# Performance work log

Hardware: AMD Instinct MI355X
Metric: run time of the kernel (lower is better)

Reference implementation:

```python
import jax, jax.numpy as jnp
import numpy as np

EMB = 1024
NH = 16
HD = EMB // NH
FF = 4 * EMB
B, T = 2, 2048
LN_EPS = 1e-5


def setup_inputs() -> dict:
    key = jax.random.key(0)
    ks = jax.random.split(key, 16)
    s = 0.02
    return {
        "x": jax.random.normal(ks[0], (B, T, EMB), jnp.float32),
        "wq": jax.random.normal(ks[1], (EMB, EMB), jnp.float32) * s,
        "bq": jnp.zeros((EMB,), jnp.float32),
        "wk": jax.random.normal(ks[2], (EMB, EMB), jnp.float32) * s,
        "bk": jnp.zeros((EMB,), jnp.float32),
        "wv": jax.random.normal(ks[3], (EMB, EMB), jnp.float32) * s,
        "bv": jnp.zeros((EMB,), jnp.float32),
        "wo": jax.random.normal(ks[4], (EMB, EMB), jnp.float32) * s,
        "bo": jnp.zeros((EMB,), jnp.float32),
        "w1": jax.random.normal(ks[5], (EMB, FF), jnp.float32) * s,
        "b1": jnp.zeros((FF,), jnp.float32),
        "w2": jax.random.normal(ks[6], (FF, EMB), jnp.float32) * s,
        "b2": jnp.zeros((EMB,), jnp.float32),
        "ln1_g": jnp.ones((EMB,), jnp.float32),
        "ln1_b": jnp.zeros((EMB,), jnp.float32),
        "ln2_g": jnp.ones((EMB,), jnp.float32),
        "ln2_b": jnp.zeros((EMB,), jnp.float32),
        "alpha_attn": jnp.float32(0.5),
        "alpha_ff": jnp.float32(0.5),
    }


def _layernorm(x, g, b):
    mu = jnp.mean(x, axis=-1, keepdims=True)
    var = jnp.var(x, axis=-1, keepdims=True)
    return (x - mu) * jax.lax.rsqrt(var + LN_EPS) * g + b


def reference(x, wq, bq, wk, bk, wv, bv, wo, bo, w1, b1, w2, b2,
              ln1_g, ln1_b, ln2_g, ln2_b, alpha_attn, alpha_ff):
    residual = x
    x_ = _layernorm(x, ln1_g, ln1_b)
    # [B,T,E] -> [B,H,T,D]
    def heads(y):
        return y.reshape(B, T, NH, HD).transpose(0, 2, 1, 3)
    q = heads(x_ @ wq + bq)
    k = heads(x_ @ wk + bk)
    v = heads(x_ @ wv + bv)
    scores = jnp.einsum("bhqd,bhkd->bhqk", q, k) / np.sqrt(HD).astype(np.float32)
    causal = jnp.tril(jnp.ones((T, T), dtype=bool))
    scores = jnp.where(causal, scores, -jnp.inf)
    attn = jax.nn.softmax(scores, axis=-1)  # dropout is identity in eval mode
    out = jnp.einsum("bhqk,bhkd->bhqd", attn, v)
    out = out.transpose(0, 2, 1, 3).reshape(B, T, EMB)
    out = out @ wo + bo
    x = residual + alpha_attn * out
    x2 = _layernorm(x, ln2_g, ln2_b)
    ff = jax.nn.gelu(x2 @ w1 + b1, approximate=False) @ w2 + b2
    return x + alpha_ff * ff
```

## Files before the change

### kernel.cpp

```cpp
#include <hip/hip_runtime.h>
#include <cmath>

#define EMB 1024
#define NH 16
#define HD 64
#define FF_DIM 4096
#define BB 2
#define TT 2048
#define NTOK (BB * TT)
#define QKVS 3072
#define SC2F 0.18033688011112042f

typedef _Float16 f16x8 __attribute__((ext_vector_type(8)));
typedef _Float16 f16x4 __attribute__((ext_vector_type(4)));
typedef float f32x4 __attribute__((ext_vector_type(4)));

__device__ __forceinline__ float gelu_fast(float x) {
    float u = x * (1.f + 0.044715f * x * x);
    float e = exp2f(u * 2.302118751f);
    return x - x / (e + 1.f);
}

template <typename TIN>
__global__ __launch_bounds__(256) void ln_kernel(const TIN* __restrict__ xin,
                                                 _Float16* __restrict__ out,
                                                 const float* __restrict__ g,
                                                 const float* __restrict__ bv) {
    int tid = threadIdx.x;
    size_t base = (size_t)blockIdx.x * EMB;
    float v[4];
#pragma unroll
    for (int i = 0; i < 4; ++i) v[i] = (float)xin[base + i * 256 + tid];
    float s = v[0] + v[1] + v[2] + v[3];
    float ss = v[0] * v[0] + v[1] * v[1] + v[2] * v[2] + v[3] * v[3];
#pragma unroll
    for (int off = 32; off > 0; off >>= 1) {
        s += __shfl_down(s, off);
        ss += __shfl_down(ss, off);
    }
    __shared__ float red[8];
    int wave = tid >> 6;
    if ((tid & 63) == 0) { red[wave] = s; red[4 + wave] = ss; }
    __syncthreads();
    s = red[0] + red[1] + red[2] + red[3];
    ss = red[4] + red[5] + red[6] + red[7];
    float mu = s * (1.0f / EMB);
    float var = ss * (1.0f / EMB) - mu * mu;
    float rstd = rsqrtf(var + 1e-5f);
#pragma unroll
    for (int i = 0; i < 4; ++i) {
        int idx = i * 256 + tid;
        float y = (v[i] - mu) * rstd * g[idx] + bv[idx];
        out[base + idx] = (_Float16)y;
    }
}

__global__ __launch_bounds__(256) void prep0_kernel(const float* __restrict__ x,
                                                    _Float16* __restrict__ xn,
                                                    const float* __restrict__ ln1_g,
                                                    const float* __restrict__ ln1_b,
                                                    const float* __restrict__ wq,
                                                    const float* __restrict__ wk,
                                                    const float* __restrict__ wv,
                                                    const float* __restrict__ wo,
                                                    const float* __restrict__ bq,
                                                    const float* __restrict__ bk,
                                                    const float* __restrict__ bv,
                                                    _Float16* __restrict__ wqkvT,
                                                    _Float16* __restrict__ woT,
                                                    float* __restrict__ qkvbias) {
    __shared__ float tile[32][33];
    int blk = blockIdx.x;
    int tid = threadIdx.x;
    if (blk >= 4108) {
        size_t base = (size_t)(blk - 4108) * EMB;
        float v[4];
#pragma unroll
        for (int i = 0; i < 4; ++i) v[i] = x[base + i * 256 + tid];
        float s = v[0] + v[1] + v[2] + v[3];
        float ss = v[0] * v[0] + v[1] * v[1] + v[2] * v[2] + v[3] * v[3];
#pragma unroll
        for (int off = 32; off > 0; off >>= 1) {
            s += __shfl_down(s, off);
            ss += __shfl_down(ss, off);
        }
        float* red = &tile[0][0];
        int wave = tid >> 6;
        if ((tid & 63) == 0) { red[wave] = s; red[4 + wave] = ss; }
        __syncthreads();
        s = red[0] + red[1] + red[2] + red[3];
        ss = red[4] + red[5] + red[6] + red[7];
        float mu = s * (1.0f / EMB);
        float var = ss * (1.0f / EMB) - mu * mu;
        float rstd = rsqrtf(var + 1e-5f);
#pragma unroll
        for (int i = 0; i < 4; ++i) {
            int idx = i * 256 + tid;
            xn[base + idx] = (_Float16)((v[i] - mu) * rstd * ln1_g[idx] + ln1_b[idx]);
        }
        return;
    }
    if (blk >= 4096) {
        int i = (blk - 4096) * 256 + tid;
        qkvbias[i] = i < 1024 ? bq[i] : (i < 2048 ? bk[i - 1024] : bv[i - 2048]);
        return;
    }
    const float* W;
    _Float16* Wt;
    int t = blk & 1023;
    int z = blk >> 10;
    if (z == 0) { W = wq; Wt = wqkvT; }
    else if (z == 1) { W = wk; Wt = wqkvT + 1024 * 1024; }
    else if (z == 2) { W = wv; Wt = wqkvT + 2 * 1024 * 1024; }
    else { W = wo; Wt = woT; }
    int bx = (t & 31) * 32, by = (t >> 5) * 32;
    int tx = tid & 31, ty = tid >> 5;
#pragma unroll
    for (int i = 0; i < 32; i += 8)
        tile[ty + i][tx] = W[(size_t)(by + ty + i) * EMB + bx + tx];
    __syncthreads();
#pragma unroll
    for (int i = 0; i < 32; i += 8)
        Wt[(size_t)(bx + ty + i) * EMB + by + tx] = (_Float16)tile[tx][ty + i];
}

__global__ __launch_bounds__(256) void prep2_kernel(const float* __restrict__ w1,
                                                    const float* __restrict__ w2,
                                                    _Float16* __restrict__ w1T,
                                                    _Float16* __restrict__ w2T) {
    int b = blockIdx.x;
    const float* W;
    _Float16* Wt;
    int K, N, t;
    if (b < 4096) { W = w1; Wt = w1T; K = 1024; N = 4096; t = b; }
    else { W = w2; Wt = w2T; K = 4096; N = 1024; t = b - 4096; }
    int ntx = N >> 5;
    int bx = (t % ntx) * 32, by = (t / ntx) * 32;
    __shared__ float tile[32][33];
    int tx = threadIdx.x & 31, ty = threadIdx.x >> 5;
#pragma unroll
    for (int i = 0; i < 32; i += 8)
        tile[ty + i][tx] = W[(size_t)(by + ty + i) * N + bx + tx];
    __syncthreads();
#pragma unroll
    for (int i = 0; i < 32; i += 8)
        Wt[(size_t)(bx + ty + i) * K + by + tx] = (_Float16)tile[tx][ty + i];
}

__global__ __launch_bounds__(256) void vT_kernel(const _Float16* __restrict__ qkv,
                                                 _Float16* __restrict__ VtG) {
    __shared__ _Float16 tile[64][72];
    int tid = threadIdx.x;
    int bh = blockIdx.y;
    int b = bh >> 4, h = bh & 15;
    int t0 = blockIdx.x * 64;
    const _Float16* src = qkv + (size_t)b * TT * QKVS + 2048 + h * HD;
    int r = tid >> 3;
    int c8 = (tid & 7) * 8;
#pragma unroll
    for (int p = 0; p < 2; ++p)
        *(f16x8*)(&tile[r + p * 32][c8]) =
            *(const f16x8*)(src + (size_t)(t0 + r + p * 32) * QKVS + c8);
    __syncthreads();
#pragma unroll
    for (int p = 0; p < 2; ++p) {
        int d = r + p * 32;
        f16x8 v;
#pragma unroll
        for (int j = 0; j < 8; ++j) v[j] = tile[c8 + j][d];
        *(f16x8*)(VtG + ((size_t)bh * HD + d) * TT + t0 + c8) = v;
    }
}

template <int MODE>
__global__ __launch_bounds__(256) void gemm_f16t(const _Float16* __restrict__ A,
                                                 const _Float16* __restrict__ Bt,
                                                 const float* __restrict__ bias,
                                                 void* __restrict__ outp,
                                                 void* __restrict__ vtg,
                                                 int M, int N, int K, int lda, int ldb) {
    __shared__ _Float16 As[128][64];
    __shared__ _Float16 Bs[128][64];
    int tid = threadIdx.x;
    int lane = tid & 63, w = tid >> 6;
    int quad = lane >> 4, l15 = lane & 15;
    int wm = (w >> 1) * 64, wn = (w & 1) * 64;
    int bM = blockIdx.y * 128, bN = blockIdx.x * 128;
    int lr = lane >> 3;
    int lcs = ((lane & 7) ^ lr) * 8;
    int sw = l15 & 7;
    f32x4 acc[4][4] = {};

    const _Float16* Abase = A + (size_t)(bM + w * 32 + lr) * lda + lcs;
    const _Float16* Bbase = Bt + (size_t)(bN + w * 32 + lr) * ldb + lcs;

    for (int kt = 0; kt < K; kt += 64) {
#pragma unroll
        for (int i = 0; i < 4; ++i) {
            __builtin_amdgcn_global_load_lds(
                (const __attribute__((address_space(1))) void*)(Abase + (size_t)(i * 8) * lda + kt),
                (__attribute__((address_space(3))) void*)(&As[w * 32 + i * 8][0]), 16, 0, 0);
            __builtin_amdgcn_global_load_lds(
                (const __attribute__((address_space(1))) void*)(Bbase + (size_t)(i * 8) * ldb + kt),
                (__attribute__((address_space(3))) void*)(&Bs[w * 32 + i * 8][0]), 16, 0, 0);
        }
        __syncthreads();
#pragma unroll
        for (int ks = 0; ks < 2; ++ks) {
            f16x8 af[4], bf[4];
#pragma unroll
            for (int i = 0; i < 4; ++i) {
                int sc = ((ks * 4 + quad) ^ sw) * 8;
                af[i] = *(const f16x8*)(&As[wm + i * 16 + l15][sc]);
                bf[i] = *(const f16x8*)(&Bs[wn + i * 16 + l15][sc]);
            }
#pragma unroll
            for (int i = 0; i < 4; ++i)
#pragma unroll
                for (int j = 0; j < 4; ++j)
                    acc[i][j] = __builtin_amdgcn_mfma_f32_16x16x32_f16(af[i], bf[j], acc[i][j], 0, 0, 0);
        }
        __syncthreads();
    }

    if (MODE == 6 && vtg != nullptr && bN >= 2048) {
        int bb = bM >> 11;
        int tbase = (bM & 2047) + wm;
#pragma unroll
        for (int i = 0; i < 4; ++i)
#pragma unroll
            for (int j = 0; j < 4; ++j) {
                int hd = bN - 2048 + wn + j * 16;
                int col = 2048 + hd + l15;
                _Float16* dst = (_Float16*)vtg +
                    (((size_t)(bb * 16 + (hd >> 6)) * 64) + (hd & 63) + l15) * TT +
                    tbase + i * 16 + quad * 4;
                f16x4 ov;
#pragma unroll
                for (int r = 0; r < 4; ++r) ov[r] = (_Float16)(acc[i][j][r] + bias[col]);
                *(f16x4*)dst = ov;
            }
        return;
    }

#pragma unroll
    for (int i = 0; i < 4; ++i)
#pragma unroll
        for (int j = 0; j < 4; ++j)
#pragma unroll
            for (int r = 0; r < 4; ++r) {
                int row = bM + wm + i * 16 + quad * 4 + r;
                int col = bN + wn + j * 16 + l15;
                size_t idx = (size_t)row * N + col;
                float vv = acc[i][j][r] + bias[col];
                if (MODE == 6) {
                    if (bN < 1024) vv *= SC2F;
                    ((_Float16*)outp)[idx] = (_Float16)vv;
                } else {
                    ((_Float16*)outp)[idx] = (_Float16)gelu_fast(vv);
                }
            }
}

#define STAGE_PAIR(OB, TN, I)                                                            \
    {                                                                                    \
        size_t ko = (size_t)(TN) * 64;                                                   \
        __builtin_amdgcn_global_load_lds(                                                \
            (const __attribute__((address_space(1))) void*)(Ab + (size_t)((I) * 8) * lda + ko), \
            (__attribute__((address_space(3))) void*)(&As[OB][w * 32 + (I) * 8][0]), 16, 0, 0); \
        __builtin_amdgcn_global_load_lds(                                                \
            (const __attribute__((address_space(1))) void*)(Bb + (size_t)((I) * 8) * ldb + ko), \
            (__attribute__((address_space(3))) void*)(&Bs[OB][w * 32 + (I) * 8][0]), 16, 0, 0); \
    }
#define RD_A(CB, I, KS) (*(const f16x8*)(&As[CB][wr * 128 + (I) * 16 + l15][(((KS)*4 + quad) ^ sw) * 8]))
#define RD_B(CB, J, KS) (*(const f16x8*)(&Bs[CB][wc * 64 + (J) * 16 + l15][(((KS)*4 + quad) ^ sw) * 8]))
#define MMQ(I0, J0)                                                                      \
    __builtin_amdgcn_s_setprio(1);                                                       \
    _Pragma("unroll") for (int ks = 0; ks < 2; ++ks) {                                   \
        _Pragma("unroll") for (int ii = 0; ii < 4; ++ii) {                               \
            _Pragma("unroll") for (int jj = 0; jj < 2; ++jj)                             \
                acc[(I0) + ii][(J0) + jj] = __builtin_amdgcn_mfma_f32_16x16x32_f16(      \
                    af[ii][ks], bf[(J0) + jj][ks], acc[(I0) + ii][(J0) + jj], 0, 0, 0);  \
        }                                                                                \
    }                                                                                    \
    __builtin_amdgcn_s_setprio(0);
#define KTILE(CB, OB, TN)                                                                \
    {                                                                                    \
                                                              \
        STAGE_PAIR(OB, TN, 0);                                                           \
        asm volatile("s_waitcnt vmcnt(2)" ::: "memory");                                 \
        __builtin_amdgcn_s_barrier();                                                    \
        _Pragma("unroll") for (int i = 0; i < 4; ++i) {                                  \
            af[i][0] = RD_A(CB, i, 0);                                                   \
            af[i][1] = RD_A(CB, i, 1);                                                   \
        }                                                                                \
        bf[0][0] = RD_B(CB, 0, 0); bf[0][1] = RD_B(CB, 0, 1);                            \
        bf[1][0] = RD_B(CB, 1, 0); bf[1][1] = RD_B(CB, 1, 1);                            \
        MMQ(0, 0);                                                                       \
        __builtin_amdgcn_s_barrier();                                                    \
                                                                            \
        bf[2][0] = RD_B(CB, 2, 0); bf[2][1] = RD_B(CB, 2, 1);                            \
        bf[3][0] = RD_B(CB, 3, 0); bf[3][1] = RD_B(CB, 3, 1);                            \
        STAGE_PAIR(OB, TN, 1);                                                           \
        __builtin_amdgcn_s_barrier();                                                    \
        MMQ(0, 2);                                                                       \
        __builtin_amdgcn_s_barrier();                                                    \
                                                                            \
        _Pragma("unroll") for (int i = 0; i < 4; ++i) {                                  \
            af[i][0] = RD_A(CB, 4 + i, 0);                                               \
            af[i][1] = RD_A(CB, 4 + i, 1);                                               \
        }                                                                                \
        STAGE_PAIR(OB, TN, 2);                                                           \
        __builtin_amdgcn_s_barrier();                                                    \
        MMQ(4, 0);                                                                       \
        __builtin_amdgcn_s_barrier();                                                    \
                                                                            \
        STAGE_PAIR(OB, TN, 3);                                                           \
        __builtin_amdgcn_s_barrier();                                                    \
        MMQ(4, 2);                                                                       \
        __builtin_amdgcn_s_barrier();                                                    \
    }

template <int MODE>
__global__ __launch_bounds__(512, 2) void gemm256(const _Float16* __restrict__ A,
                                                  const _Float16* __restrict__ Bt,
                                                  const float* __restrict__ bias,
                                                  void* __restrict__ outp,
                                                  void* __restrict__ vtg,
                                                  int M, int N, int K, int lda, int ldb) {
    __shared__ _Float16 As[2][256][64];
    __shared__ _Float16 Bs[2][256][64];
    int tid = threadIdx.x;
    int lane = tid & 63, w = tid >> 6;
    int quad = lane >> 4, l15 = lane & 15;
    int wr = w >> 2, wc = w & 3;
    int gx = gridDim.x;
    int nwg = gx * gridDim.y;
    int bid = blockIdx.y * gx + blockIdx.x;
    int cpx = nwg >> 3;
    int sbid = (bid & 7) * cpx + (bid >> 3);
    int bN = (sbid % gx) * 256;
    int bM = (sbid / gx) * 256;
    int lr = lane >> 3;
    int lcs = ((lane & 7) ^ lr) * 8;
    int sw = l15 & 7;
    f32x4 acc[8][4] = {};
    f16x8 af[4][2], bf[4][2];

    const _Float16* Ab = A + (size_t)(bM + w * 32 + lr) * lda + lcs;
    const _Float16* Bb = Bt + (size_t)(bN + w * 32 + lr) * ldb + lcs;
    const int NT = K >> 6;

#pragma unroll
    for (int i = 0; i < 4; ++i) STAGE_PAIR(0, 0, i);

    for (int it = 0; it < NT; it += 2) {
        int tn1 = it + 1;
        int tn2 = (it + 2 < NT) ? it + 2 : 0;
        KTILE(0, 1, tn1);
        KTILE(1, 0, tn2);
    }

    if (MODE == 1 && vtg != nullptr && bN >= 2048) {
        int bb = bM >> 11;
#pragma unroll
        for (int i = 0; i < 8; ++i)
#pragma unroll
            for (int j = 0; j < 4; ++j) {
                int hd = bN - 2048 + wc * 64 + j * 16;
                int col = 2048 + hd + l15;
                int tb = (bM & 2047) + wr * 128 + i * 16 + quad * 4;
                _Float16* dst = (_Float16*)vtg +
                    (((size_t)(bb * 16 + (hd >> 6)) * 64) + (hd & 63) + l15) * TT + tb;
                f16x4 ov;
#pragma unroll
                for (int r = 0; r < 4; ++r) ov[r] = (_Float16)(acc[i][j][r] + bias[col]);
                *(f16x4*)dst = ov;
            }
        return;
    }

#pragma unroll
    for (int i = 0; i < 8; ++i)
#pragma unroll
        for (int j = 0; j < 4; ++j)
#pragma unroll
            for (int r = 0; r < 4; ++r) {
                int row = bM + wr * 128 + i * 16 + quad * 4 + r;
                int col = bN + wc * 64 + j * 16 + l15;
                size_t idx = (size_t)row * N + col;
                float vv = acc[i][j][r] + bias[col];
                if (MODE == 1) {
                    if (bN < 1024) vv *= SC2F;
                    ((_Float16*)outp)[idx] = (_Float16)vv;
                } else {
                    ((_Float16*)outp)[idx] = (_Float16)gelu_fast(vv);
                }
            }
}

template <int MODE>
__global__ __launch_bounds__(256) void gemm64(const _Float16* __restrict__ A,
                                              const _Float16* __restrict__ Bt,
                                              const float* __restrict__ bias,
                                              void* __restrict__ outp,
                                              const void* __restrict__ residp,
                                              const float* __restrict__ alphap,
                                              int M, int N, int K, int lda, int ldb) {
    __shared__ _Float16 As[128][64];
    __shared__ _Float16 Bs[64][64];
    int tid = threadIdx.x;
    int lane = tid & 63, w = tid >> 6;
    int quad = lane >> 4, l15 = lane & 15;
    int wm = w * 32;
    int bM = blockIdx.y * 128, bN = blockIdx.x * 64;
    int lr = lane >> 3;
    int lcs = ((lane & 7) ^ lr) * 8;
    int sw = l15 & 7;
    int kz = (MODE == 7) ? blockIdx.z * K : 0;
    f32x4 acc[2][4] = {};

    const _Float16* Abase = A + (size_t)(bM + w * 32 + lr) * lda + kz + lcs;
    const _Float16* Bbase = Bt + (size_t)(bN + w * 16 + lr) * ldb + kz + lcs;

    for (int kt = 0; kt < K; kt += 64) {
#pragma unroll
        for (int i = 0; i < 4; ++i)
            __builtin_amdgcn_global_load_lds(
                (const __attribute__((address_space(1))) void*)(Abase + (size_t)(i * 8) * lda + kt),
                (__attribute__((address_space(3))) void*)(&As[w * 32 + i * 8][0]), 16, 0, 0);
#pragma unroll
        for (int i = 0; i < 2; ++i)
            __builtin_amdgcn_global_load_lds(
                (const __attribute__((address_space(1))) void*)(Bbase + (size_t)(i * 8) * ldb + kt),
                (__attribute__((address_space(3))) void*)(&Bs[w * 16 + i * 8][0]), 16, 0, 0);
        __syncthreads();
#pragma unroll
        for (int ks = 0; ks < 2; ++ks) {
            int sc = ((ks * 4 + quad) ^ sw) * 8;
            f16x8 af[2], bf[4];
#pragma unroll
            for (int i = 0; i < 2; ++i)
                af[i] = *(const f16x8*)(&As[wm + i * 16 + l15][sc]);
#pragma unroll
            for (int j = 0; j < 4; ++j)
                bf[j] = *(const f16x8*)(&Bs[j * 16 + l15][sc]);
#pragma unroll
            for (int i = 0; i < 2; ++i)
#pragma unroll
                for (int j = 0; j < 4; ++j)
                    acc[i][j] = __builtin_amdgcn_mfma_f32_16x16x32_f16(af[i], bf[j], acc[i][j], 0, 0, 0);
        }
        __syncthreads();
    }

    float alpha = 0.f;
    if (MODE == 2 || MODE == 5) alpha = alphap[0];
    _Float16* pout = nullptr;
    if (MODE == 7) pout = blockIdx.z ? (_Float16*)(void*)residp : (_Float16*)outp;
#pragma unroll
    for (int i = 0; i < 2; ++i)
#pragma unroll
        for (int j = 0; j < 4; ++j)
#pragma unroll
            for (int r = 0; r < 4; ++r) {
                int row = bM + wm + i * 16 + quad * 4 + r;
                int col = bN + j * 16 + l15;
                size_t idx = (size_t)row * N + col;
                if (MODE == 7) {
                    pout[idx] = (_Float16)acc[i][j][r];
                } else if (MODE == 4) {
                    ((float*)outp)[idx] = acc[i][j][r];
                } else if (MODE == 2) {
                    float vv = acc[i][j][r] + bias[col];
                    float rsd = ((const float*)residp)[idx];
                    ((_Float16*)outp)[idx] = (_Float16)(rsd + alpha * vv);
                } else {
                    float vv = acc[i][j][r] + bias[col];
                    float prev = ((float*)outp)[idx];
                    float rsd = (float)((const _Float16*)residp)[idx];
                    ((float*)outp)[idx] = rsd + alpha * (prev + vv);
                }
            }
}

__global__ __launch_bounds__(256) void ff2_reduce_kernel(const _Float16* __restrict__ p0,
                                                         const _Float16* __restrict__ p1,
                                                         const _Float16* __restrict__ xmid,
                                                         const float* __restrict__ b2,
                                                         const float* __restrict__ alphap,
                                                         float* __restrict__ out) {
    int i = (blockIdx.x * 256 + threadIdx.x) * 8;
    float alpha = alphap[0];
    f16x8 a = *(const f16x8*)(p0 + i);
    f16x8 b = *(const f16x8*)(p1 + i);
    f16x8 xm = *(const f16x8*)(xmid + i);
    int col = i & 1023;
#pragma unroll
    for (int k = 0; k < 8; ++k)
        out[i + k] = (float)xm[k] + alpha * ((float)a[k] + (float)b[k] + b2[col + k]);
}

#define QT 64
#define NEG_BIG (-1e30f)
__global__ __launch_bounds__(512) void attn_mfma_kernel(const _Float16* __restrict__ qkv,
                                                        const _Float16* __restrict__ VtG,
                                                        _Float16* __restrict__ O) {
    __shared__ _Float16 Ks[64][72];
    __shared__ _Float16 Vt[64][72];
    __shared__ _Float16 Ps[8][16][68];
    int tid = threadIdx.x;
    int lane = tid & 63, w = tid >> 6;
    int quad = lane >> 4, l15 = lane & 15;
    int bh = blockIdx.x;
    int b = bh >> 4, h = bh & 15;
    int y = blockIdx.y;
    int seg = w >> 2, ws = w & 3;
    int qt = seg ? y : (31 - y);
    int q0 = qt * QT;
    int ntw = qt + 1;
    int ntmax = 32 - y;
    const _Float16* Qh = qkv + (size_t)b * TT * QKVS + h * HD;
    const _Float16* Kh = Qh + 1024;
    const _Float16* Vrows = VtG + (size_t)bh * HD * TT;

    int m0 = q0 + ws * 16;
    f16x8 aq0 = *(const f16x8*)(Qh + (size_t)(m0 + l15) * QKVS + quad * 8);
    f16x8 aq1 = *(const f16x8*)(Qh + (size_t)(m0 + l15) * QKVS + 32 + quad * 8);

    f32x4 Oacc[4] = {};
    float lrow[4] = {0.f, 0.f, 0.f, 0.f};

    int rr = tid >> 3;
    int c8 = (tid & 7) * 8;
    const _Float16* Kp = Kh + (size_t)rr * QKVS + c8;
    const _Float16* Vp = Vrows + (size_t)rr * TT + c8;

    f16x8 kreg = *(const f16x8*)(Kp);
    f16x8 vreg = *(const f16x8*)(Vp);

    for (int t = 0; t < ntmax; ++t) {
        int t0 = t * 64;
        __syncthreads();
        *(f16x8*)(&Ks[rr][c8]) = kreg;
        *(f16x8*)(&Vt[rr][c8]) = vreg;
        __syncthreads();
        if (t + 1 < ntmax) {
            kreg = *(const f16x8*)(Kp + (size_t)(t0 + 64) * QKVS);
            vreg = *(const f16x8*)(Vp + t0 + 64);
        }
        if (t >= ntw) continue;

        f32x4 Sacc[4] = {};
        __builtin_amdgcn_s_setprio(1);
#pragma unroll
        for (int nc = 0; nc < 4; ++nc) {
            f16x8 bk0 = *(const f16x8*)(&Ks[nc * 16 + l15][quad * 8]);
            f16x8 bk1 = *(const f16x8*)(&Ks[nc * 16 + l15][32 + quad * 8]);
            Sacc[nc] = __builtin_amdgcn_mfma_f32_16x16x32_f16(aq0, bk0, Sacc[nc], 0, 0, 0);
            Sacc[nc] = __builtin_amdgcn_mfma_f32_16x16x32_f16(aq1, bk1, Sacc[nc], 0, 0, 0);
        }
        __builtin_amdgcn_s_setprio(0);

        if (t0 == q0) {
#pragma unroll
            for (int nc = 0; nc < 4; ++nc) {
                int key = t0 + nc * 16 + l15;
#pragma unroll
                for (int i = 0; i < 4; ++i)
                    if (key > m0 + quad * 4 + i) Sacc[nc][i] = NEG_BIG;
            }
        }

#pragma unroll
        for (int nc = 0; nc < 4; ++nc)
#pragma unroll
            for (int i = 0; i < 4; ++i) {
                float p = exp2f(Sacc[nc][i]);
                lrow[i] += p;
                Ps[w][quad * 4 + i][nc * 16 + l15] = (_Float16)p;
            }
        __asm__ __volatile__("s_waitcnt lgkmcnt(0)" ::: "memory");

        f16x8 ap0 = *(const f16x8*)(&Ps[w][l15][quad * 8]);
        f16x8 ap1 = *(const f16x8*)(&Ps[w][l15][32 + quad * 8]);
        __builtin_amdgcn_s_setprio(1);
#pragma unroll
        for (int nc = 0; nc < 4; ++nc) {
            int d = nc * 16 + l15;
            f16x8 bv0 = *(const f16x8*)(&Vt[d][quad * 8]);
            f16x8 bv1 = *(const f16x8*)(&Vt[d][32 + quad * 8]);
            Oacc[nc] = __builtin_amdgcn_mfma_f32_16x16x32_f16(ap0, bv0, Oacc[nc], 0, 0, 0);
            Oacc[nc] = __builtin_amdgcn_mfma_f32_16x16x32_f16(ap1, bv1, Oacc[nc], 0, 0, 0);
        }
        __builtin_amdgcn_s_setprio(0);
    }

#pragma unroll
    for (int off = 1; off < 16; off <<= 1)
#pragma unroll
        for (int i = 0; i < 4; ++i) lrow[i] += __shfl_xor(lrow[i], off);
#pragma unroll
    for (int i = 0; i < 4; ++i) lrow[i] = 1.0f / lrow[i];
    _Float16* Oh = O + (size_t)b * TT * EMB + h * HD;
#pragma unroll
    for (int nc = 0; nc < 4; ++nc)
#pragma unroll
        for (int i = 0; i < 4; ++i) {
            int row = m0 + quad * 4 + i;
            Oh[(size_t)row * EMB + nc * 16 + l15] = (_Float16)(Oacc[nc][i] * lrow[i]);
        }
}

extern "C" void kernel_launch(void* const* d_in, const int* in_sizes, int n_in,
                              void* d_out, int out_size, void* d_ws, size_t ws_size,
                              hipStream_t stream) {
    const float* x = (const float*)d_in[0];
    const float* wq = (const float*)d_in[1];
    const float* bq = (const float*)d_in[2];
    const float* wk = (const float*)d_in[3];
    const float* bk = (const float*)d_in[4];
    const float* wv = (const float*)d_in[5];
    const float* bv = (const float*)d_in[6];
    const float* wo = (const float*)d_in[7];
    const float* bo = (const float*)d_in[8];
    const float* w1 = (const float*)d_in[9];
    const float* b1 = (const float*)d_in[10];
    const float* w2 = (const float*)d_in[11];
    const float* b2 = (const float*)d_in[12];
    const float* ln1_g = (const float*)d_in[13];
    const float* ln1_b = (const float*)d_in[14];
    const float* ln2_g = (const float*)d_in[15];
    const float* ln2_b = (const float*)d_in[16];
    const float* alpha_attn = (const float*)d_in[17];
    const float* alpha_ff = (const float*)d_in[18];

    const size_t SL = (size_t)8 * 1024 * 1024;
    char* ws = (char*)d_ws;
    _Float16* xn = (_Float16*)(ws);
    _Float16* qkv = (_Float16*)(ws + SL);
    _Float16* wqkvT = (_Float16*)(ws + 4 * SL);
    float* qkvbias = (float*)(ws + 4 * SL + 6 * 1024 * 1024);
    _Float16* attnout = (_Float16*)(ws);
    _Float16* xmid = (_Float16*)(ws + SL);
    _Float16* x2 = (_Float16*)(ws + 2 * SL);
    _Float16* w1T = (_Float16*)(ws);
    _Float16* w2T = (_Float16*)(ws + 3 * SL);
    _Float16* ff1 = (_Float16*)(ws + 4 * SL);
    bool bigws = ws_size >= (size_t)64 * 1024 * 1024;
    _Float16* VtG = bigws ? (_Float16*)(ws + 5 * SL) : (_Float16*)(ws + 4 * SL);
    _Float16* woT = bigws ? (_Float16*)(ws + 6 * SL) : (_Float16*)(ws + 5 * SL);
    _Float16* part0 = (_Float16*)(ws);
    _Float16* part1 = (_Float16*)(ws + 2 * SL);

    prep0_kernel<<<8204, 256, 0, stream>>>(x, xn, ln1_g, ln1_b, wq, wk, wv, wo,
                                           bq, bk, bv, wqkvT, woT, qkvbias);

    if (bigws) {
        gemm256<1><<<dim3(QKVS / 256, NTOK / 256), 512, 0, stream>>>(
            xn, wqkvT, qkvbias, qkv, (void*)VtG, NTOK, QKVS, EMB, EMB, EMB);
    } else {
        gemm_f16t<6><<<dim3(QKVS / 128, NTOK / 128), 256, 0, stream>>>(
            xn, wqkvT, qkvbias, qkv, nullptr, NTOK, QKVS, EMB, EMB, EMB);
        vT_kernel<<<dim3(TT / 64, BB * NH), 256, 0, stream>>>(qkv, VtG);
    }

    attn_mfma_kernel<<<dim3(BB * NH, TT / QT / 2), 512, 0, stream>>>(qkv, VtG, attnout);

    gemm64<2><<<dim3(EMB / 64, NTOK / 128), 256, 0, stream>>>(
        attnout, woT, bo, xmid, x, alpha_attn, NTOK, EMB, EMB, EMB, EMB);

    ln_kernel<_Float16><<<NTOK, 256, 0, stream>>>(xmid, x2, ln2_g, ln2_b);

    prep2_kernel<<<8192, 256, 0, stream>>>(w1, w2, w1T, w2T);

    if (bigws) {
        gemm256<0><<<dim3(FF_DIM / 256, NTOK / 256), 512, 0, stream>>>(
            x2, w1T, b1, ff1, nullptr, NTOK, FF_DIM, EMB, EMB, EMB);
        gemm64<7><<<dim3(EMB / 64, NTOK / 128, 2), 256, 0, stream>>>(
            ff1, w2T, nullptr, part0, part1, nullptr, NTOK, EMB, 2048, FF_DIM, FF_DIM);
        ff2_reduce_kernel<<<NTOK * EMB / 8 / 256, 256, 0, stream>>>(
            part0, part1, xmid, b2, alpha_ff, (float*)d_out);
    } else {
        const int NC = 2048;
        for (int hh = 0; hh < 2; ++hh) {
            const _Float16* w1Th = w1T + (size_t)hh * NC * EMB;
            const _Float16* w2Th = w2T + (size_t)hh * NC;
            gemm_f16t<1><<<dim3(NC / 128, NTOK / 128), 256, 0, stream>>>(
                x2, w1Th, b1 + hh * NC, ff1, nullptr, NTOK, NC, EMB, EMB, EMB);
            if (hh == 0)
                gemm64<4><<<dim3(EMB / 64, NTOK / 128), 256, 0, stream>>>(
                    ff1, w2Th, nullptr, d_out, nullptr, nullptr, NTOK, EMB, NC, NC, FF_DIM);
            else
                gemm64<5><<<dim3(EMB / 64, NTOK / 128), 256, 0, stream>>>(
                    ff1, w2Th, b2, d_out, xmid, alpha_ff, NTOK, EMB, NC, NC, FF_DIM);
        }
    }
}
```

Measured before the change: 366.3 us.

## Replace interleaved ping-pong GEMM schedule with simple double-buffered loop

Replaces the hand-interleaved K-tile schedule, which split staging into four pairs with barriers between MFMA quarters and raised wave priority with setprio, with a plain double-buffered loop. Each iteration now issues all four staging loads for the next tile up front, runs all MFMAs on the current buffer, then waits for all loads and synchronises once. This removes many barriers per tile and the priority toggling. In exchange it gives up the fine-grained interleaving of loads with compute and waits on vmcnt(0) each tile, which may expose more memory latency.

```diff
diff --git a/kernel.cpp b/kernel.cpp
--- a/kernel.cpp
+++ b/kernel.cpp
@@ -275,50 +275,12 @@
 #define RD_A(CB, I, KS) (*(const f16x8*)(&As[CB][wr * 128 + (I) * 16 + l15][(((KS)*4 + quad) ^ sw) * 8]))
 #define RD_B(CB, J, KS) (*(const f16x8*)(&Bs[CB][wc * 64 + (J) * 16 + l15][(((KS)*4 + quad) ^ sw) * 8]))
 #define MMQ(I0, J0)                                                                      \
-    __builtin_amdgcn_s_setprio(1);                                                       \
     _Pragma("unroll") for (int ks = 0; ks < 2; ++ks) {                                   \
         _Pragma("unroll") for (int ii = 0; ii < 4; ++ii) {                               \
             _Pragma("unroll") for (int jj = 0; jj < 2; ++jj)                             \
                 acc[(I0) + ii][(J0) + jj] = __builtin_amdgcn_mfma_f32_16x16x32_f16(      \
                     af[ii][ks], bf[(J0) + jj][ks], acc[(I0) + ii][(J0) + jj], 0, 0, 0);  \
         }                                                                                \
-    }                                                                                    \
-    __builtin_amdgcn_s_setprio(0);
-#define KTILE(CB, OB, TN)                                                                \
-    {                                                                                    \
-                                                              \
-        STAGE_PAIR(OB, TN, 0);                                                           \
-        asm volatile("s_waitcnt vmcnt(2)" ::: "memory");                                 \
-        __builtin_amdgcn_s_barrier();                                                    \
-        _Pragma("unroll") for (int i = 0; i < 4; ++i) {                                  \
-            af[i][0] = RD_A(CB, i, 0);                                                   \
-            af[i][1] = RD_A(CB, i, 1);                                                   \
-        }                                                                                \
-        bf[0][0] = RD_B(CB, 0, 0); bf[0][1] = RD_B(CB, 0, 1);                            \
-        bf[1][0] = RD_B(CB, 1, 0); bf[1][1] = RD_B(CB, 1, 1);                            \
-        MMQ(0, 0);                                                                       \
-        __builtin_amdgcn_s_barrier();                                                    \
-                                                                            \
-        bf[2][0] = RD_B(CB, 2, 0); bf[2][1] = RD_B(CB, 2, 1);                            \
-        bf[3][0] = RD_B(CB, 3, 0); bf[3][1] = RD_B(CB, 3, 1);                            \
-        STAGE_PAIR(OB, TN, 1);                                                           \
-        __builtin_amdgcn_s_barrier();                                                    \
-        MMQ(0, 2);                                                                       \
-        __builtin_amdgcn_s_barrier();                                                    \
-                                                                            \
-        _Pragma("unroll") for (int i = 0; i < 4; ++i) {                                  \
-            af[i][0] = RD_A(CB, 4 + i, 0);                                               \
-            af[i][1] = RD_A(CB, 4 + i, 1);                                               \
-        }                                                                                \
-        STAGE_PAIR(OB, TN, 2);                                                           \
-        __builtin_amdgcn_s_barrier();                                                    \
-        MMQ(4, 0);                                                                       \
-        __builtin_amdgcn_s_barrier();                                                    \
-                                                                            \
-        STAGE_PAIR(OB, TN, 3);                                                           \
-        __builtin_amdgcn_s_barrier();                                                    \
-        MMQ(4, 2);                                                                       \
-        __builtin_amdgcn_s_barrier();                                                    \
     }
 
 template <int MODE>
@@ -353,12 +315,36 @@
 
 #pragma unroll
     for (int i = 0; i < 4; ++i) STAGE_PAIR(0, 0, i);
-
-    for (int it = 0; it < NT; it += 2) {
-        int tn1 = it + 1;
-        int tn2 = (it + 2 < NT) ? it + 2 : 0;
-        KTILE(0, 1, tn1);
-        KTILE(1, 0, tn2);
+    asm volatile("s_waitcnt vmcnt(0)" ::: "memory");
+    __builtin_amdgcn_s_barrier();
+
+    int cur = 0;
+    for (int t = 0; t < NT; ++t) {
+        int nxt = cur ^ 1;
+        int tn = (t + 1 < NT) ? t + 1 : 0;
+#pragma unroll
+        for (int i = 0; i < 4; ++i) STAGE_PAIR(nxt, tn, i);
+#pragma unroll
+        for (int i = 0; i < 4; ++i) {
+            af[i][0] = RD_A(cur, i, 0);
+            af[i][1] = RD_A(cur, i, 1);
+        }
+        bf[0][0] = RD_B(cur, 0, 0); bf[0][1] = RD_B(cur, 0, 1);
+        bf[1][0] = RD_B(cur, 1, 0); bf[1][1] = RD_B(cur, 1, 1);
+        MMQ(0, 0);
+        bf[2][0] = RD_B(cur, 2, 0); bf[2][1] = RD_B(cur, 2, 1);
+        bf[3][0] = RD_B(cur, 3, 0); bf[3][1] = RD_B(cur, 3, 1);
+        MMQ(0, 2);
+#pragma unroll
+        for (int i = 0; i < 4; ++i) {
+            af[i][0] = RD_A(cur, 4 + i, 0);
+            af[i][1] = RD_A(cur, 4 + i, 1);
+        }
+        MMQ(4, 0);
+        MMQ(4, 2);
+        asm volatile("s_waitcnt vmcnt(0)" ::: "memory");
+        __builtin_amdgcn_s_barrier();
+        cur = nxt;
     }
 
     if (MODE == 1 && vtg != nullptr && bN >= 2048) {
```

Result: faster. 358.2 us (-2.2%).
